# Performance work log

Hardware: AMD Instinct MI355X
Metric: run time of the kernel (lower is better)

## Reference

```python
import jax, jax.numpy as jnp
import numpy as np

N_CHILDS = 50000
N_EDGES = 500000
NODE_FEAT = 256
NUM_SEM = 57
HID = 256
EDGE_FEAT = 64
EDGE_TYPES = 4
NUM_ITERS = 2


def setup_inputs() -> dict:
    key = jax.random.key(0)
    ks = jax.random.split(key, 12)
    d_in = NODE_FEAT + NUM_SEM            # 313
    d_ne = 2 * HID + EDGE_FEAT + EDGE_TYPES  # 580
    d_par = HID * (NUM_ITERS + 1)         # 768
    def lin(k, fan_in, fan_out):
        kw, kb = jax.random.split(k)
        s = 1.0 / np.sqrt(fan_in)
        return (jax.random.uniform(kw, (fan_in, fan_out), jnp.float32, -s, s),
                jax.random.uniform(kb, (fan_out,), jnp.float32, -s, s))
    W_child, b_child = lin(ks[0], d_in, HID)
    W_ne0, b_ne0 = lin(ks[1], d_ne, HID)
    W_ne1, b_ne1 = lin(ks[2], d_ne, HID)
    W_parent, b_parent = lin(ks[3], d_par, NODE_FEAT)
    return {
        "child_feats": jax.random.normal(ks[4], (1, N_CHILDS, d_in), jnp.float32),
        "child_exists": jnp.ones((1, N_CHILDS, 1), jnp.float32),
        "edge_type_onehot": jax.random.normal(ks[5], (1, N_EDGES, EDGE_TYPES), jnp.float32),
        "edge_feats": jax.random.normal(ks[6], (1, N_EDGES, EDGE_FEAT), jnp.float32),
        "edge_indices": jax.random.randint(ks[7], (1, N_EDGES, 2), 0, N_CHILDS, jnp.int64),
        "W_child": W_child, "b_child": b_child,
        "W_ne0": W_ne0, "b_ne0": b_ne0,
        "W_ne1": W_ne1, "b_ne1": b_ne1,
        "W_parent": W_parent, "b_parent": b_parent,
    }


def reference(child_feats, child_exists, edge_type_onehot, edge_feats, edge_indices,
              W_child, b_child, W_ne0, b_ne0, W_ne1, b_ne1, W_parent, b_parent):
    n = child_feats.shape[1]
    # node embedding: linear + relu, mask non-existent children
    x = jax.nn.relu(jnp.einsum('bnd,dh->bnh', child_feats, W_child) + b_child)
    x = x * child_exists                              # [1, N, H]
    iter_parent = [x.max(axis=1)]                     # symmetric_type == 'max'
    ef = jnp.concatenate([edge_type_onehot, edge_feats], axis=2)[0]  # [E, 4+64]
    src = edge_indices[0, :, 0]
    dst = edge_indices[0, :, 1]
    cnt = jax.ops.segment_sum(jnp.ones((src.shape[0],), x.dtype), src, num_segments=n)
    denom = jnp.maximum(cnt, 1.0)[:, None]            # scatter_mean clamp
    for W, b in ((W_ne0, b_ne0), (W_ne1, b_ne1)):
        nef = jnp.concatenate([x[0, src], x[0, dst], ef], axis=1)  # [E, 580]
        nef = jax.nn.relu(nef @ W + b)                # [E, H]
        # edge_symmetric_type == 'avg': scatter_mean over source index
        x = (jax.ops.segment_sum(nef, src, num_segments=n) / denom)[None]
        iter_parent.append(x.max(axis=1))
    parent = jnp.concatenate(iter_parent, axis=1)     # [1, H*(iters+1)]
    return jax.nn.relu(parent @ W_parent + b_parent)  # [1, node_feat_size]
```

## Files before the change

### kernel.cpp

```cpp
#include <hip/hip_runtime.h>

#define NC   50000
#define NE   500000
#define DIN  313
#define DNE  580
#define KPC  320
#define KB   96
#define NB_SCAN 196

typedef __attribute__((ext_vector_type(8))) short bf16x8;
typedef __attribute__((ext_vector_type(4))) float f32x4;

static __device__ __forceinline__ unsigned short f2bf(float f) {
    unsigned u = __float_as_uint(f);
    unsigned r = (u + 0x7fff + ((u >> 16) & 1)) >> 16;
    return (unsigned short)r;
}
static __device__ __forceinline__ float bf2f(unsigned short u) {
    return __uint_as_float(((unsigned)u) << 16);
}
static __device__ __forceinline__ void gload_lds16(const unsigned short* g, unsigned short* l) {
    __builtin_amdgcn_global_load_lds(
        (const __attribute__((address_space(1))) unsigned int*)(g),
        (__attribute__((address_space(3))) unsigned int*)(l), 16, 0, 0);
}

__global__ __launch_bounds__(256) void prep_w_kernel(
    const float* __restrict__ W0, const float* __restrict__ W1,
    const float* __restrict__ Wc,
    unsigned short* __restrict__ Wpt, unsigned short* __restrict__ Wbt,
    unsigned short* __restrict__ Wct)
{
    int b = blockIdx.x;
    if (b < 1024) {
        int layer = b >> 9, n2 = b & 511;
        const float* W = layer ? W1 : W0;
        unsigned short* dst = Wpt + (size_t)layer * 512 * 256 + (size_t)n2 * 256;
        int t = threadIdx.x;
        int ch = t >> 5, s = (t >> 3) & 3, j = t & 7;
        int gk = ch * 32 + ((s ^ (n2 & 3)) * 8) + j;
        float v = (n2 < 256) ? W[(size_t)gk * 256 + n2] : W[(size_t)(256 + gk) * 256 + (n2 - 256)];
        dst[t] = f2bf(v);
    } else if (b < 1536) {
        int idx = b - 1024;
        int layer = idx >> 8, n = idx & 255;
        const float* W = layer ? W1 : W0;
        unsigned short* dst = Wbt + (size_t)layer * 256 * KB + (size_t)n * KB;
        int t = threadIdx.x;
        if (t < KB) {
            int ch = t >> 5, s = (t >> 3) & 3, j = t & 7;
            int gk = ch * 32 + ((s ^ (n & 3)) * 8) + j;
            float v = (512 + gk < DNE) ? W[(size_t)(512 + gk) * 256 + n] : 0.0f;
            dst[t] = f2bf(v);
        }
    } else {
        int n = b - 1536;
        unsigned short* dst = Wct + (size_t)n * KPC;
        for (int t = threadIdx.x; t < KPC; t += 256) {
            int ch = t >> 5, s = (t >> 3) & 3, j = t & 7;
            int gk = ch * 32 + ((s ^ (n & 3)) * 8) + j;
            float v = (gk < DIN) ? Wc[(size_t)gk * 256 + n] : 0.0f;
            dst[t] = f2bf(v);
        }
    }
}

__global__ __launch_bounds__(256, 4) void child_mfma_kernel(
    const float* __restrict__ cf, const float* __restrict__ exists,
    const unsigned short* __restrict__ Wct, const float* __restrict__ bias,
    unsigned short* __restrict__ xb, float* __restrict__ pmax)
{
    __shared__ unsigned short sA[64][40];
    __shared__ unsigned short sB[256][32];
    __shared__ float smax[256];

    const int tid = threadIdx.x, lane = tid & 63, wid = tid >> 6;
    const int wm = wid >> 1, wn = wid & 1, l15 = lane & 15, l4 = lane >> 4;
    const int node0 = blockIdx.x * 64;
    const int arow = tid >> 2, s3 = tid & 3;

    smax[tid] = 0.0f;

    f32x4 acc[2][8];
    #pragma unroll
    for (int mi = 0; mi < 2; ++mi)
        #pragma unroll
        for (int ni = 0; ni < 8; ++ni)
            acc[mi][ni] = (f32x4){0.f, 0.f, 0.f, 0.f};

    int nodeA = node0 + arow; if (nodeA >= NC) nodeA = NC - 1;

    for (int ch = 0; ch < 10; ++ch) {
        #pragma unroll
        for (int i = 0; i < 4; ++i) {
            int n = (wid << 6) + (i << 4) + (lane >> 2);
            gload_lds16(Wct + (size_t)n * KPC + ch * 32 + (lane & 3) * 8,
                        &sB[(wid << 6) + (i << 4)][0]);
        }
        {
            int gk0 = ch * 32 + s3 * 8;
            union { unsigned short u[8]; int4 v; } pk;
            #pragma unroll
            for (int j = 0; j < 8; ++j) {
                int gk = gk0 + j;
                float f = (gk < DIN) ? cf[(size_t)nodeA * DIN + gk] : 0.0f;
                pk.u[j] = f2bf(f);
            }
            *(int4*)&sA[arow][s3 * 8] = pk.v;
        }
        __syncthreads();
        bf16x8 af[2];
        #pragma unroll
        for (int mi = 0; mi < 2; ++mi)
            af[mi] = *(const bf16x8*)&sA[wm * 32 + mi * 16 + l15][l4 * 8];
        #pragma unroll
        for (int ni = 0; ni < 8; ++ni) {
            int n = wn * 128 + ni * 16 + l15;
            bf16x8 bfr = *(const bf16x8*)&sB[n][(l4 ^ (n & 3)) * 8];
            acc[0][ni] = __builtin_amdgcn_mfma_f32_16x16x32_bf16(af[0], bfr, acc[0][ni], 0, 0, 0);
            acc[1][ni] = __builtin_amdgcn_mfma_f32_16x16x32_bf16(af[1], bfr, acc[1][ni], 0, 0, 0);
        }
        __syncthreads();
    }

    float bv[8];
    #pragma unroll
    for (int ni = 0; ni < 8; ++ni) bv[ni] = bias[wn * 128 + ni * 16 + l15];
    float cmax[8];
    #pragma unroll
    for (int ni = 0; ni < 8; ++ni) cmax[ni] = 0.0f;

    #pragma unroll
    for (int mi = 0; mi < 2; ++mi) {
        #pragma unroll
        for (int r = 0; r < 4; ++r) {
            int node = node0 + wm * 32 + mi * 16 + l4 * 4 + r;
            if (node < NC) {
                float ex = exists[node];
                #pragma unroll
                for (int ni = 0; ni < 8; ++ni) {
                    float v = fmaxf(acc[mi][ni][r] + bv[ni], 0.f) * ex;
                    xb[(size_t)node * 256 + wn * 128 + ni * 16 + l15] = f2bf(v);
                    cmax[ni] = fmaxf(cmax[ni], v);
                }
            }
        }
    }
    #pragma unroll
    for (int ni = 0; ni < 8; ++ni)
        atomicMax((unsigned int*)&smax[wn * 128 + ni * 16 + l15], __float_as_uint(cmax[ni]));
    __syncthreads();
    atomicMax((unsigned int*)&pmax[tid], __float_as_uint(smax[tid]));
}

__global__ __launch_bounds__(256, 3) void node_gemm_kernel(
    const unsigned short* __restrict__ xb,
    const unsigned short* __restrict__ Wpt,
    unsigned short* __restrict__ yp)
{
    __shared__ unsigned short sA[2][64][40];
    __shared__ unsigned short sB[2][256][32];

    const int tid = threadIdx.x, lane = tid & 63, wid = tid >> 6;
    const int wm = wid >> 1, wn = wid & 1, l15 = lane & 15, l4 = lane >> 4;
    const int node0 = blockIdx.x * 64;
    const int n0 = blockIdx.y * 256;
    const int arow = tid >> 2, s3 = tid & 3;

    int nodeA = node0 + arow; if (nodeA >= NC) nodeA = NC - 1;

    f32x4 acc[2][8];
    #pragma unroll
    for (int mi = 0; mi < 2; ++mi)
        #pragma unroll
        for (int ni = 0; ni < 8; ++ni)
            acc[mi][ni] = (f32x4){0.f, 0.f, 0.f, 0.f};

    #pragma unroll
    for (int i = 0; i < 4; ++i) {
        int n = (wid << 6) + (i << 4) + (lane >> 2);
        gload_lds16(Wpt + (size_t)(n0 + n) * 256 + (lane & 3) * 8, &sB[0][(wid << 6) + (i << 4)][0]);
    }
    *(int4*)&sA[0][arow][s3 * 8] = *(const int4*)(xb + (size_t)nodeA * 256 + s3 * 8);
    __syncthreads();

    int buf = 0;
    for (int ch = 0; ch < 8; ++ch) {
        const int nch = ch + 1;
        int4 areg;
        if (nch < 8) {
            #pragma unroll
            for (int i = 0; i < 4; ++i) {
                int n = (wid << 6) + (i << 4) + (lane >> 2);
                gload_lds16(Wpt + (size_t)(n0 + n) * 256 + nch * 32 + (lane & 3) * 8,
                            &sB[buf ^ 1][(wid << 6) + (i << 4)][0]);
            }
            areg = *(const int4*)(xb + (size_t)nodeA * 256 + nch * 32 + s3 * 8);
        }
        bf16x8 af[2];
        #pragma unroll
        for (int mi = 0; mi < 2; ++mi)
            af[mi] = *(const bf16x8*)&sA[buf][wm * 32 + mi * 16 + l15][l4 * 8];
        #pragma unroll
        for (int ni = 0; ni < 8; ++ni) {
            int n = wn * 128 + ni * 16 + l15;
            bf16x8 bfr = *(const bf16x8*)&sB[buf][n][(l4 ^ (n & 3)) * 8];
            acc[0][ni] = __builtin_amdgcn_mfma_f32_16x16x32_bf16(af[0], bfr, acc[0][ni], 0, 0, 0);
            acc[1][ni] = __builtin_amdgcn_mfma_f32_16x16x32_bf16(af[1], bfr, acc[1][ni], 0, 0, 0);
        }
        if (nch < 8) *(int4*)&sA[buf ^ 1][arow][s3 * 8] = areg;
        __syncthreads();
        buf ^= 1;
    }

    #pragma unroll
    for (int mi = 0; mi < 2; ++mi) {
        #pragma unroll
        for (int r = 0; r < 4; ++r) {
            int node = node0 + wm * 32 + mi * 16 + l4 * 4 + r;
            if (node < NC) {
                #pragma unroll
                for (int ni = 0; ni < 8; ++ni)
                    yp[(size_t)node * 512 + n0 + wn * 128 + ni * 16 + l15] = f2bf(acc[mi][ni][r]);
            }
        }
    }
}

__global__ __launch_bounds__(256) void count_int_kernel(
    const int* __restrict__ eidx, int* __restrict__ icnt)
{
    int t = blockIdx.x * 256 + threadIdx.x;
    if (t < NE) atomicAdd(&icnt[eidx[2 * t]], 1);
}

__global__ __launch_bounds__(256) void scan1_kernel(
    const int* __restrict__ icnt, int* __restrict__ part)
{
    __shared__ int sd[256];
    int i = blockIdx.x * 256 + threadIdx.x;
    sd[threadIdx.x] = (i < NC) ? icnt[i] : 0;
    __syncthreads();
    for (int d = 128; d > 0; d >>= 1) {
        if (threadIdx.x < d) sd[threadIdx.x] += sd[threadIdx.x + d];
        __syncthreads();
    }
    if (threadIdx.x == 0) part[blockIdx.x] = sd[0];
}

__global__ void scan2_kernel(int* __restrict__ part)
{
    if (threadIdx.x == 0) {
        int acc = 0;
        for (int i = 0; i < NB_SCAN; ++i) { int v = part[i]; part[i] = acc; acc += v; }
    }
}

__global__ __launch_bounds__(256) void scan3_kernel(
    const int* __restrict__ icnt, const int* __restrict__ part,
    int* __restrict__ cur)
{
    __shared__ int sc[256];
    const int t = threadIdx.x;
    int i = blockIdx.x * 256 + t;
    int val = (i < NC) ? icnt[i] : 0;
    sc[t] = val;
    __syncthreads();
    for (int d = 1; d < 256; d <<= 1) {
        int x = (t >= d) ? sc[t - d] : 0;
        __syncthreads();
        sc[t] += x;
        __syncthreads();
    }
    if (i < NC) cur[i] = part[blockIdx.x] + sc[t] - val;
}

__global__ __launch_bounds__(256) void bin_kernel(
    const int* __restrict__ eidx, int* __restrict__ cur, int* __restrict__ perm)
{
    int t = blockIdx.x * 256 + threadIdx.x;
    if (t < NE) {
        int s = eidx[2 * t];
        int p = atomicAdd(&cur[s], 1);
        perm[p] = t;
    }
}

__global__ __launch_bounds__(256) void inv_kernel(
    const int* __restrict__ icnt, float* __restrict__ inv)
{
    int t = blockIdx.x * 256 + threadIdx.x;
    if (t < NC) inv[t] = 1.0f / fmaxf((float)icnt[t], 1.0f);
}

__global__ __launch_bounds__(256, 3) void combine_kernel(
    const unsigned short* __restrict__ yp,
    const float* __restrict__ eto, const float* __restrict__ efe,
    const int* __restrict__ eidx, const int* __restrict__ perm,
    const unsigned short* __restrict__ Wbt,
    const float* __restrict__ bias,
    float* __restrict__ accb)
{
    __shared__ unsigned short sA[3][64][40];
    __shared__ unsigned short sW[2][256][32];
    __shared__ int s_src[64], s_dst[64], s_perm[64];

    const int tid = threadIdx.x;
    const int nwg = gridDim.x;
    const int q = nwg >> 3, rr = nwg & 7;
    const int xcd = blockIdx.x & 7, within = blockIdx.x >> 3;
    const int bid = (xcd < rr ? xcd * (q + 1) : rr * (q + 1) + (xcd - rr) * q) + within;
    const int e0 = bid * 64;

    if (tid < 64) {
        int ee = e0 + tid; if (ee >= NE) ee = NE - 1;
        int e = perm[ee];
        s_perm[tid] = e;
        s_src[tid] = eidx[2 * e];
        s_dst[tid] = eidx[2 * e + 1];
    }
    const int lane = tid & 63;
    const int wid  = tid >> 6;
    const int wm   = wid >> 1;
    const int wn   = wid & 1;
    const int l15  = lane & 15;
    const int l4   = lane >> 4;
    const int arow = tid >> 2;
    const int s3   = tid & 3;

    f32x4 acc[2][8];
    #pragma unroll
    for (int mi = 0; mi < 2; ++mi)
        #pragma unroll
        for (int ni = 0; ni < 8; ++ni)
            acc[mi][ni] = (f32x4){0.f, 0.f, 0.f, 0.f};

    #pragma unroll
    for (int i = 0; i < 4; ++i) {
        int n = (wid << 6) + (i << 4) + (lane >> 2);
        gload_lds16(Wbt + (size_t)n * KB + (lane & 3) * 8, &sW[0][(wid << 6) + (i << 4)][0]);
    }
    __syncthreads();

    const int my_e = s_perm[arow];
    #pragma unroll
    for (int ch = 0; ch < 3; ++ch) {
        int g0 = ch * 32 + s3 * 8;
        union { unsigned short u[8]; int4 v; } pk;
        #pragma unroll
        for (int j = 0; j < 8; ++j) {
            int g = g0 + j;
            float f = 0.0f;
            if (g < 4)       f = eto[(size_t)my_e * 4 + g];
            else if (g < 68) f = efe[(size_t)my_e * 64 + (g - 4)];
            pk.u[j] = f2bf(f);
        }
        *(int4*)&sA[ch][arow][s3 * 8] = pk.v;
    }
    __syncthreads();

    int buf = 0;
    #pragma unroll
    for (int ch = 0; ch < 3; ++ch) {
        if (ch + 1 < 3) {
            #pragma unroll
            for (int i = 0; i < 4; ++i) {
                int n = (wid << 6) + (i << 4) + (lane >> 2);
                gload_lds16(Wbt + (size_t)n * KB + (ch + 1) * 32 + (lane & 3) * 8,
                            &sW[buf ^ 1][(wid << 6) + (i << 4)][0]);
            }
        }
        bf16x8 af[2];
        #pragma unroll
        for (int mi = 0; mi < 2; ++mi)
            af[mi] = *(const bf16x8*)&sA[ch][wm * 32 + mi * 16 + l15][l4 * 8];
        #pragma unroll
        for (int ni = 0; ni < 8; ++ni) {
            int n = wn * 128 + ni * 16 + l15;
            bf16x8 bfr = *(const bf16x8*)&sW[buf][n][(l4 ^ (n & 3)) * 8];
            acc[0][ni] = __builtin_amdgcn_mfma_f32_16x16x32_bf16(af[0], bfr, acc[0][ni], 0, 0, 0);
            acc[1][ni] = __builtin_amdgcn_mfma_f32_16x16x32_bf16(af[1], bfr, acc[1][ni], 0, 0, 0);
        }
        __syncthreads();
        buf ^= 1;
    }

    float (*ep)[258] = (float (*)[258])(&sW[0][0][0]);
    const int col = tid;
    const float b_col = bias[col];

    int curn = s_src[0];
    int rstart = 0;
    float run = 0.f;
    #pragma unroll
    for (int c = 0; c < 4; ++c) {
        if (wm == (c >> 1)) {
            const int mi = c & 1;
            #pragma unroll
            for (int ni = 0; ni < 8; ++ni) {
                #pragma unroll
                for (int r = 0; r < 4; ++r)
                    ep[l4 * 4 + r][wn * 128 + ni * 16 + l15] = acc[mi][ni][r];
            }
        }
        float yt[16], ym[16];
        #pragma unroll
        for (int r = 0; r < 16; ++r) {
            int row = c * 16 + r;
            yt[r] = bf2f(yp[(size_t)s_src[row] * 512 + col]);
            ym[r] = bf2f(yp[(size_t)s_dst[row] * 512 + 256 + col]);
        }
        __syncthreads();
        #pragma unroll
        for (int r = 0; r < 16; ++r) {
            int row = c * 16 + r;
            float v = 0.0f;
            if (e0 + row < NE)
                v = fmaxf(ep[r][col] + yt[r] + ym[r] + b_col, 0.f);
            int sr = s_src[row];
            if (sr != curn) {
                if (rstart > 0) accb[(size_t)curn * 256 + col] = run;
                else            atomicAdd(&accb[(size_t)curn * 256 + col], run);
                curn = sr; run = v; rstart = row;
            } else {
                run += v;
            }
        }
        __syncthreads();
    }
    atomicAdd(&accb[(size_t)curn * 256 + col], run);
}

__global__ __launch_bounds__(256) void finalize_kernel(
    const float* __restrict__ src, const float* __restrict__ inv,
    unsigned short* __restrict__ xb_out, float* __restrict__ pmax, int n)
{
    const int tid = threadIdx.x;
    int i0 = blockIdx.x * 128;
    int iend = i0 + 128; if (iend > n) iend = n;
    float m = 0.0f;
    for (int i = i0; i < iend; ++i) {
        float v = src[(size_t)i * 256 + tid];
        v *= inv[i];
        xb_out[(size_t)i * 256 + tid] = f2bf(v);
        m = fmaxf(m, v);
    }
    atomicMax((unsigned int*)&pmax[tid], __float_as_uint(m));
}

__global__ __launch_bounds__(256) void parent_kernel(
    const float* __restrict__ pmax, const float* __restrict__ W,
    const float* __restrict__ bias, float* __restrict__ out)
{
    __shared__ float sp[768];
    const int tid = threadIdx.x;
    for (int i = tid; i < 768; i += 256) sp[i] = pmax[i];
    __syncthreads();
    float s = bias[tid];
    for (int k = 0; k < 768; ++k) s = fmaf(sp[k], W[(size_t)k * 256 + tid], s);
    out[tid] = fmaxf(s, 0.f);
}

extern "C" void kernel_launch(void* const* d_in, const int* in_sizes, int n_in,
                              void* d_out, int out_size, void* d_ws, size_t ws_size,
                              hipStream_t stream)
{
    const float* cf   = (const float*)d_in[0];
    const float* ex   = (const float*)d_in[1];
    const float* eto  = (const float*)d_in[2];
    const float* efe  = (const float*)d_in[3];
    const int*   eidx = (const int*)d_in[4];
    const float* Wc   = (const float*)d_in[5];
    const float* bc   = (const float*)d_in[6];
    const float* W0   = (const float*)d_in[7];
    const float* b0   = (const float*)d_in[8];
    const float* W1   = (const float*)d_in[9];
    const float* b1   = (const float*)d_in[10];
    const float* Wp   = (const float*)d_in[11];
    const float* bp   = (const float*)d_in[12];

    float*          accb = (float*)d_ws;
    float*          invv = accb + (size_t)NC * 256;
    float*          pmax = invv + NC;
    unsigned short* xb   = (unsigned short*)(pmax + 768);
    unsigned short* yp   = xb + (size_t)NC * 256;
    unsigned short* Wpt  = yp + (size_t)NC * 512;
    unsigned short* Wbt  = Wpt + (size_t)2 * 512 * 256;
    unsigned short* Wct  = Wbt + (size_t)2 * 256 * KB;
    int*            icnt = (int*)(Wct + (size_t)256 * KPC);
    int*            part = icnt + NC;
    int*            curb = part + 256;
    int*            perm = curb + NC;

    hipMemsetAsync(pmax, 0, 768 * sizeof(float), stream);
    hipMemsetAsync(icnt, 0, NC * sizeof(int), stream);

    prep_w_kernel<<<1792, 256, 0, stream>>>(W0, W1, Wc, Wpt, Wbt, Wct);
    child_mfma_kernel<<<(NC + 63) / 64, 256, 0, stream>>>(cf, ex, Wct, bc, xb, pmax);

    count_int_kernel<<<(NE + 255) / 256, 256, 0, stream>>>(eidx, icnt);
    scan1_kernel<<<NB_SCAN, 256, 0, stream>>>(icnt, part);
    scan2_kernel<<<1, 64, 0, stream>>>(part);
    scan3_kernel<<<NB_SCAN, 256, 0, stream>>>(icnt, part, curb);
    bin_kernel<<<(NE + 255) / 256, 256, 0, stream>>>(eidx, curb, perm);
    inv_kernel<<<(NC + 255) / 256, 256, 0, stream>>>(icnt, invv);

    for (int it = 0; it < 2; ++it) {
        node_gemm_kernel<<<dim3((NC + 63) / 64, 2), 256, 0, stream>>>(
            xb, Wpt + (size_t)it * 512 * 256, yp);
        hipMemsetAsync(accb, 0, (size_t)NC * 256 * sizeof(float), stream);
        combine_kernel<<<(NE + 63) / 64, 256, 0, stream>>>(
            yp, eto, efe, eidx, perm, Wbt + (size_t)it * 256 * KB, it ? b1 : b0, accb);
        finalize_kernel<<<(NC + 127) / 128, 256, 0, stream>>>(accb, invv, xb, pmax + 256 * (it + 1), NC);
    }
    parent_kernel<<<1, 256, 0, stream>>>(pmax, Wp, bp, (float*)d_out);
}
```

Measured before the change: 696.2 us.

## Load combine-kernel edge weights directly from global into registers, shrink LDS

The combine kernel no longer stages the 256x96 edge-feature weight slice through double-buffered shared memory. Each wave now reads its B fragments straight from global memory (L2-resident, unswizzled layout) into registers, and the A tile and epilogue buffer share one aliased LDS region. This drops the per-chunk barriers and the LDS footprint, and launch bounds are raised to 4 blocks per CU for more occupancy. In exchange, weight fragments are refetched from cache by every block and wave, and registers may be tighter at the higher occupancy target.

```diff
diff --git a/kernel.cpp b/kernel.cpp
--- a/kernel.cpp
+++ b/kernel.cpp
@@ -48,9 +48,7 @@
         unsigned short* dst = Wbt + (size_t)layer * 256 * KB + (size_t)n * KB;
         int t = threadIdx.x;
         if (t < KB) {
-            int ch = t >> 5, s = (t >> 3) & 3, j = t & 7;
-            int gk = ch * 32 + ((s ^ (n & 3)) * 8) + j;
-            float v = (512 + gk < DNE) ? W[(size_t)(512 + gk) * 256 + n] : 0.0f;
+            float v = (512 + t < DNE) ? W[(size_t)(512 + t) * 256 + n] : 0.0f;
             dst[t] = f2bf(v);
         }
     } else {
@@ -293,7 +291,7 @@
     if (t < NC) inv[t] = 1.0f / fmaxf((float)icnt[t], 1.0f);
 }
 
-__global__ __launch_bounds__(256, 3) void combine_kernel(
+__global__ __launch_bounds__(256, 4) void combine_kernel(
     const unsigned short* __restrict__ yp,
     const float* __restrict__ eto, const float* __restrict__ efe,
     const int* __restrict__ eidx, const int* __restrict__ perm,
@@ -301,8 +299,9 @@
     const float* __restrict__ bias,
     float* __restrict__ accb)
 {
-    __shared__ unsigned short sA[3][64][40];
-    __shared__ unsigned short sW[2][256][32];
+    __shared__ __align__(16) unsigned char smemraw[16 * 258 * 4];
+    unsigned short (*sA)[64][40] = (unsigned short (*)[64][40])smemraw;
+    float (*ep)[258] = (float (*)[258])smemraw;
     __shared__ int s_src[64], s_dst[64], s_perm[64];
 
     const int tid = threadIdx.x;
@@ -328,18 +327,6 @@
     const int arow = tid >> 2;
     const int s3   = tid & 3;
 
-    f32x4 acc[2][8];
-    #pragma unroll
-    for (int mi = 0; mi < 2; ++mi)
-        #pragma unroll
-        for (int ni = 0; ni < 8; ++ni)
-            acc[mi][ni] = (f32x4){0.f, 0.f, 0.f, 0.f};
-
-    #pragma unroll
-    for (int i = 0; i < 4; ++i) {
-        int n = (wid << 6) + (i << 4) + (lane >> 2);
-        gload_lds16(Wbt + (size_t)n * KB + (lane & 3) * 8, &sW[0][(wid << 6) + (i << 4)][0]);
-    }
     __syncthreads();
 
     const int my_e = s_perm[arow];
@@ -359,33 +346,30 @@
     }
     __syncthreads();
 
-    int buf = 0;
+    f32x4 acc[2][8];
+    #pragma unroll
+    for (int mi = 0; mi < 2; ++mi)
+        #pragma unroll
+        for (int ni = 0; ni < 8; ++ni)
+            acc[mi][ni] = (f32x4){0.f, 0.f, 0.f, 0.f};
+
+    const unsigned short* wp = Wbt + (size_t)(wn * 128 + l15) * KB + l4 * 8;
     #pragma unroll
     for (int ch = 0; ch < 3; ++ch) {
-        if (ch + 1 < 3) {
-            #pragma unroll
-            for (int i = 0; i < 4; ++i) {
-                int n = (wid << 6) + (i << 4) + (lane >> 2);
-                gload_lds16(Wbt + (size_t)n * KB + (ch + 1) * 32 + (lane & 3) * 8,
-                            &sW[buf ^ 1][(wid << 6) + (i << 4)][0]);
-            }
-        }
-        bf16x8 af[2];
-        #pragma unroll
-        for (int mi = 0; mi < 2; ++mi)
-            af[mi] = *(const bf16x8*)&sA[ch][wm * 32 + mi * 16 + l15][l4 * 8];
+        bf16x8 bw[8];
+        #pragma unroll
+        for (int ni = 0; ni < 8; ++ni)
+            bw[ni] = *(const bf16x8*)(wp + (size_t)ni * 16 * KB + ch * 32);
+        bf16x8 af0 = *(const bf16x8*)&sA[ch][wm * 32 + l15][l4 * 8];
+        bf16x8 af1 = *(const bf16x8*)&sA[ch][wm * 32 + 16 + l15][l4 * 8];
         #pragma unroll
         for (int ni = 0; ni < 8; ++ni) {
-            int n = wn * 128 + ni * 16 + l15;
-            bf16x8 bfr = *(const bf16x8*)&sW[buf][n][(l4 ^ (n & 3)) * 8];
-            acc[0][ni] = __builtin_amdgcn_mfma_f32_16x16x32_bf16(af[0], bfr, acc[0][ni], 0, 0, 0);
-            acc[1][ni] = __builtin_amdgcn_mfma_f32_16x16x32_bf16(af[1], bfr, acc[1][ni], 0, 0, 0);
-        }
-        __syncthreads();
-        buf ^= 1;
-    }
-
-    float (*ep)[258] = (float (*)[258])(&sW[0][0][0]);
+            acc[0][ni] = __builtin_amdgcn_mfma_f32_16x16x32_bf16(af0, bw[ni], acc[0][ni], 0, 0, 0);
+            acc[1][ni] = __builtin_amdgcn_mfma_f32_16x16x32_bf16(af1, bw[ni], acc[1][ni], 0, 0, 0);
+        }
+    }
+    __syncthreads();
+
     const int col = tid;
     const float b_col = bias[col];
 
```

Measured after the change: 720.8 us. 3.5% more time.

## Pre-pack permuted edge features to bf16 once and reuse across iterations

Applied to the files above, without the earlier changes.

Adds a prep kernel that gathers edge type and edge features in sorted (perm) order, converts them to bf16 in an MFMA-ready chunked layout, and stores sorted src/dst indices. The combine kernel then loads A tiles directly with global_load_lds instead of gathering and converting fp32 features through perm on every iteration. This aims to cut the random fp32 gather traffic and conversion work in both combine passes, at the cost of one extra pass and extra workspace. The old path is kept as a fallback when the workspace is too small.

```diff
diff --git a/kernel.cpp b/kernel.cpp
--- a/kernel.cpp
+++ b/kernel.cpp
@@ -2,6 +2,7 @@
 
 #define NC   50000
 #define NE   500000
+#define NEP  (NE + 64)
 #define DIN  313
 #define DNE  580
 #define KPC  320
@@ -293,7 +294,181 @@
     if (t < NC) inv[t] = 1.0f / fmaxf((float)icnt[t], 1.0f);
 }
 
-__global__ __launch_bounds__(256, 3) void combine_kernel(
+__global__ __launch_bounds__(256) void ef_prep_kernel(
+    const float* __restrict__ eto, const float* __restrict__ efe,
+    const int* __restrict__ perm, const int* __restrict__ eidx,
+    unsigned short* __restrict__ efc01, unsigned short* __restrict__ efc2,
+    int* __restrict__ esrc, int* __restrict__ edst)
+{
+    int p = blockIdx.x * 256 + threadIdx.x;
+    if (p >= NE) return;
+    int e = perm[p];
+    esrc[p] = eidx[2 * e];
+    edst[p] = eidx[2 * e + 1];
+    const float* efr = efe + (size_t)e * 64;
+
+    union { unsigned short u[8]; int4 v; } pk;
+    {
+        float4 a = *(const float4*)(eto + (size_t)e * 4);
+        float4 b = *(const float4*)(efr + 0);
+        pk.u[0]=f2bf(a.x); pk.u[1]=f2bf(a.y); pk.u[2]=f2bf(a.z); pk.u[3]=f2bf(a.w);
+        pk.u[4]=f2bf(b.x); pk.u[5]=f2bf(b.y); pk.u[6]=f2bf(b.z); pk.u[7]=f2bf(b.w);
+        *(int4*)(efc01 + (size_t)p * 32) = pk.v;
+    }
+    #pragma unroll
+    for (int g = 1; g < 4; ++g) {
+        float4 a = *(const float4*)(efr + g * 8 - 4);
+        float4 b = *(const float4*)(efr + g * 8);
+        pk.u[0]=f2bf(a.x); pk.u[1]=f2bf(a.y); pk.u[2]=f2bf(a.z); pk.u[3]=f2bf(a.w);
+        pk.u[4]=f2bf(b.x); pk.u[5]=f2bf(b.y); pk.u[6]=f2bf(b.z); pk.u[7]=f2bf(b.w);
+        *(int4*)(efc01 + (size_t)p * 32 + g * 8) = pk.v;
+    }
+    #pragma unroll
+    for (int g = 0; g < 4; ++g) {
+        float4 a = *(const float4*)(efr + 28 + g * 8);
+        float4 b = *(const float4*)(efr + 32 + g * 8);
+        pk.u[0]=f2bf(a.x); pk.u[1]=f2bf(a.y); pk.u[2]=f2bf(a.z); pk.u[3]=f2bf(a.w);
+        pk.u[4]=f2bf(b.x); pk.u[5]=f2bf(b.y); pk.u[6]=f2bf(b.z); pk.u[7]=f2bf(b.w);
+        *(int4*)(efc01 + ((size_t)NEP + p) * 32 + g * 8) = pk.v;
+    }
+    {
+        float4 a = *(const float4*)(efr + 60);
+        pk.u[0]=f2bf(a.x); pk.u[1]=f2bf(a.y); pk.u[2]=f2bf(a.z); pk.u[3]=f2bf(a.w);
+        pk.u[4]=0; pk.u[5]=0; pk.u[6]=0; pk.u[7]=0;
+        *(int4*)(efc2 + (size_t)p * 8) = pk.v;
+    }
+}
+
+__global__ __launch_bounds__(256, 3) void combine_efc_kernel(
+    const unsigned short* __restrict__ yp,
+    const unsigned short* __restrict__ efc01,
+    const unsigned short* __restrict__ efc2,
+    const int* __restrict__ esrc, const int* __restrict__ edst,
+    const unsigned short* __restrict__ Wbt,
+    const float* __restrict__ bias,
+    float* __restrict__ accb)
+{
+    __shared__ unsigned short sA01[2][64][32];
+    __shared__ unsigned short sA2[64][8];
+    __shared__ unsigned short sW[2][256][32];
+    __shared__ int s_src[64], s_dst[64];
+
+    const int tid = threadIdx.x;
+    const int nwg = gridDim.x;
+    const int q = nwg >> 3, rr = nwg & 7;
+    const int xcd = blockIdx.x & 7, within = blockIdx.x >> 3;
+    const int bid = (xcd < rr ? xcd * (q + 1) : rr * (q + 1) + (xcd - rr) * q) + within;
+    const int e0 = bid * 64;
+
+    const int lane = tid & 63;
+    const int wid  = tid >> 6;
+    const int wm   = wid >> 1;
+    const int wn   = wid & 1;
+    const int l15  = lane & 15;
+    const int l4   = lane >> 4;
+
+    if (tid < 64) {
+        int e = e0 + tid; if (e > NE - 1) e = NE - 1;
+        s_src[tid] = esrc[e];
+        s_dst[tid] = edst[e];
+    }
+    #pragma unroll
+    for (int i = 0; i < 4; ++i) {
+        gload_lds16(Wbt + (size_t)((wid << 6) + (i << 4) + (lane >> 2)) * KB + (lane & 3) * 8,
+                    &sW[0][(wid << 6) + (i << 4)][0]);
+    }
+    gload_lds16(efc01 + ((size_t)e0 + wid * 16) * 32 + lane * 8, &sA01[0][wid * 16][0]);
+    gload_lds16(efc01 + ((size_t)NEP + e0 + wid * 16) * 32 + lane * 8, &sA01[1][wid * 16][0]);
+    if (wid == 0)
+        gload_lds16(efc2 + (size_t)e0 * 8 + lane * 8, &sA2[0][0]);
+    __syncthreads();
+
+    f32x4 acc[2][8];
+    #pragma unroll
+    for (int mi = 0; mi < 2; ++mi)
+        #pragma unroll
+        for (int ni = 0; ni < 8; ++ni)
+            acc[mi][ni] = (f32x4){0.f, 0.f, 0.f, 0.f};
+
+    int buf = 0;
+    #pragma unroll
+    for (int ch = 0; ch < 3; ++ch) {
+        if (ch + 1 < 3) {
+            #pragma unroll
+            for (int i = 0; i < 4; ++i) {
+                gload_lds16(Wbt + (size_t)((wid << 6) + (i << 4) + (lane >> 2)) * KB + (ch + 1) * 32 + (lane & 3) * 8,
+                            &sW[buf ^ 1][(wid << 6) + (i << 4)][0]);
+            }
+        }
+        bf16x8 af0, af1;
+        if (ch < 2) {
+            af0 = *(const bf16x8*)&sA01[ch][wm * 32 + l15][l4 * 8];
+            af1 = *(const bf16x8*)&sA01[ch][wm * 32 + 16 + l15][l4 * 8];
+        } else {
+            bf16x8 z = (bf16x8){0,0,0,0,0,0,0,0};
+            bf16x8 a0 = *(const bf16x8*)&sA2[wm * 32 + l15][0];
+            bf16x8 a1 = *(const bf16x8*)&sA2[wm * 32 + 16 + l15][0];
+            af0 = (l4 == 0) ? a0 : z;
+            af1 = (l4 == 0) ? a1 : z;
+        }
+        #pragma unroll
+        for (int ni = 0; ni < 8; ++ni) {
+            int n = wn * 128 + ni * 16 + l15;
+            bf16x8 bfr = *(const bf16x8*)&sW[buf][n][(l4 ^ (n & 3)) * 8];
+            acc[0][ni] = __builtin_amdgcn_mfma_f32_16x16x32_bf16(af0, bfr, acc[0][ni], 0, 0, 0);
+            acc[1][ni] = __builtin_amdgcn_mfma_f32_16x16x32_bf16(af1, bfr, acc[1][ni], 0, 0, 0);
+        }
+        __syncthreads();
+        buf ^= 1;
+    }
+
+    float (*ep)[258] = (float (*)[258])(&sW[0][0][0]);
+    const int col = tid;
+    const float b_col = bias[col];
+
+    int curn = s_src[0];
+    int rstart = 0;
+    float run = 0.f;
+    #pragma unroll
+    for (int c = 0; c < 4; ++c) {
+        if (wm == (c >> 1)) {
+            const int mi = c & 1;
+            #pragma unroll
+            for (int ni = 0; ni < 8; ++ni) {
+                #pragma unroll
+                for (int r = 0; r < 4; ++r)
+                    ep[l4 * 4 + r][wn * 128 + ni * 16 + l15] = acc[mi][ni][r];
+            }
+        }
+        float yt[16], ym[16];
+        #pragma unroll
+        for (int r = 0; r < 16; ++r) {
+            int row = c * 16 + r;
+            yt[r] = bf2f(yp[(size_t)s_src[row] * 512 + col]);
+            ym[r] = bf2f(yp[(size_t)s_dst[row] * 512 + 256 + col]);
+        }
+        __syncthreads();
+        #pragma unroll
+        for (int r = 0; r < 16; ++r) {
+            int row = c * 16 + r;
+            float v = 0.0f;
+            if (e0 + row < NE)
+                v = fmaxf(ep[r][col] + yt[r] + ym[r] + b_col, 0.f);
+            int sr = s_src[row];
+            if (sr != curn) {
+                if (rstart > 0) accb[(size_t)curn * 256 + col] = run;
+                else            atomicAdd(&accb[(size_t)curn * 256 + col], run);
+                curn = sr; run = v; rstart = row;
+            } else {
+                run += v;
+            }
+        }
+        __syncthreads();
+    }
+    atomicAdd(&accb[(size_t)curn * 256 + col], run);
+}
+
+__global__ __launch_bounds__(256, 3) void combine_f32_kernel(
     const unsigned short* __restrict__ yp,
     const float* __restrict__ eto, const float* __restrict__ efe,
     const int* __restrict__ eidx, const int* __restrict__ perm,
@@ -491,6 +666,12 @@
     int*            part = icnt + NC;
     int*            curb = part + 256;
     int*            perm = curb + NC;
+    unsigned short* efc01 = (unsigned short*)(perm + NE);
+    unsigned short* efc2  = efc01 + (size_t)2 * NEP * 32;
+    int*            esrc  = (int*)(efc2 + (size_t)NEP * 8);
+    int*            edst  = esrc + NE;
+    size_t need = (size_t)((char*)(edst + NE) - (char*)d_ws);
+    const bool use_efc = (ws_size >= need);
 
     hipMemsetAsync(pmax, 0, 768 * sizeof(float), stream);
     hipMemsetAsync(icnt, 0, NC * sizeof(int), stream);
@@ -504,13 +685,22 @@
     scan3_kernel<<<NB_SCAN, 256, 0, stream>>>(icnt, part, curb);
     bin_kernel<<<(NE + 255) / 256, 256, 0, stream>>>(eidx, curb, perm);
     inv_kernel<<<(NC + 255) / 256, 256, 0, stream>>>(icnt, invv);
-
+    if (use_efc)
+        ef_prep_kernel<<<(NE + 255) / 256, 256, 0, stream>>>(eto, efe, perm, eidx, efc01, efc2, esrc, edst);
+
+    const int nwg = (NE + 63) / 64;
     for (int it = 0; it < 2; ++it) {
         node_gemm_kernel<<<dim3((NC + 63) / 64, 2), 256, 0, stream>>>(
             xb, Wpt + (size_t)it * 512 * 256, yp);
         hipMemsetAsync(accb, 0, (size_t)NC * 256 * sizeof(float), stream);
-        combine_kernel<<<(NE + 63) / 64, 256, 0, stream>>>(
-            yp, eto, efe, eidx, perm, Wbt + (size_t)it * 256 * KB, it ? b1 : b0, accb);
+        if (use_efc)
+            combine_efc_kernel<<<nwg, 256, 0, stream>>>(
+                yp, efc01, efc2, esrc, edst,
+                Wbt + (size_t)it * 256 * KB, it ? b1 : b0, accb);
+        else
+            combine_f32_kernel<<<nwg, 256, 0, stream>>>(
+                yp, eto, efe, eidx, perm,
+                Wbt + (size_t)it * 256 * KB, it ? b1 : b0, accb);
         finalize_kernel<<<(NC + 127) / 128, 256, 0, stream>>>(accb, invv, xb, pmax + 256 * (it + 1), NC);
     }
     parent_kernel<<<1, 256, 0, stream>>>(pmax, Wp, bp, (float*)d_out);
```

After: 726.0 us. +4.3%, slower.
